# Kernel tuning notes

Hardware: AMD Instinct MI355X
Metric: run time of the kernel (lower is better)

Reference implementation:

```python
import jax, jax.numpy as jnp
import numpy as np

B_, N, C, H = 8192, 49, 192, 6
HD = C // H
SCALE = HD ** -0.5


def setup_inputs() -> dict:
    key = jax.random.key(0)
    k0, k1, k2, k3 = jax.random.split(key, 4)
    x = jax.random.normal(k0, (B_, N, C), dtype=jnp.float32)
    mask = jax.random.randint(k1, (B_, N), 0, 2, dtype=jnp.int32)
    w_qkv = jax.random.normal(k2, (C, 3 * C), dtype=jnp.float32) * 0.02
    b_qkv = jnp.zeros((3 * C,), dtype=jnp.float32)
    w_proj = jax.random.normal(k3, (C, C), dtype=jnp.float32) * 0.02
    b_proj = jnp.zeros((C,), dtype=jnp.float32)
    return {"x": x, "mask": mask, "w_qkv": w_qkv, "b_qkv": b_qkv,
            "w_proj": w_proj, "b_proj": b_proj}


def reference(x, mask, w_qkv, b_qkv, w_proj, b_proj):
    # qkv projection: [B_, N, 3C] -> [3, B_, H, N, HD]
    qkv = (x @ w_qkv + b_qkv).reshape(B_, N, 3, H, HD).transpose(2, 0, 3, 1, 4)
    q, k, v = qkv[0], qkv[1], qkv[2]
    # scaled QK^T: [B_, H, N, N]
    attn = jnp.einsum('bhnd,bhmd->bhnm', q, k) * SCALE
    # additive key mask: mask==0 positions get -inf
    attn = jnp.where(mask[:, None, None, :] == 0, -jnp.inf, attn)
    p = jax.nn.softmax(attn, axis=-1)  # dropout p=0 -> identity
    out = jnp.einsum('bhnm,bhmd->bhnd', p, v)  # AV
    out = out.transpose(0, 2, 1, 3).reshape(B_, N, C)
    return out @ w_proj + b_proj
```

## Files before the change

kernel.cpp:

```cpp
#include <hip/hip_runtime.h>


typedef __attribute__((ext_vector_type(8))) short short8;
typedef __attribute__((ext_vector_type(4))) float f32x4;

#define SCALE 0.17677669529663687f

__device__ __forceinline__ unsigned short f2bf(float x) {
    union { float f; unsigned int i; } v; v.f = x;
    return (unsigned short)((v.i + 0x7FFFu + ((v.i >> 16) & 1u)) >> 16);
}

__device__ __forceinline__ unsigned int pkbf(float lo, float hi) {
    unsigned int r;
    asm("v_cvt_pk_bf16_f32 %0, %1, %2" : "=v"(r) : "v"(lo), "v"(hi));
    return r;
}

__device__ __forceinline__ short8 cvt8(f32x4 lo, f32x4 hi) {
    union { short8 s; unsigned int u[4]; } r;
    r.u[0] = pkbf(lo[0], lo[1]);
    r.u[1] = pkbf(lo[2], lo[3]);
    r.u[2] = pkbf(hi[0], hi[1]);
    r.u[3] = pkbf(hi[2], hi[3]);
    return r.s;
}

__device__ __forceinline__ f32x4 addb(f32x4 v, float b) {
    v[0] += b; v[1] += b; v[2] += b; v[3] += b;
    return v;
}

__device__ __forceinline__ short8 xpose(f32x4 tlo, f32x4 thi, int srcA, bool hi) {
    unsigned int pl0 = pkbf(tlo[0], tlo[1]);
    unsigned int pl1 = pkbf(tlo[2], tlo[3]);
    unsigned int ph0 = pkbf(thi[0], thi[1]);
    unsigned int ph1 = pkbf(thi[2], thi[3]);
    unsigned int a0 = (unsigned int)__shfl((int)pl0, srcA);
    unsigned int b0 = (unsigned int)__shfl((int)ph0, srcA);
    unsigned int a1 = (unsigned int)__shfl((int)pl1, srcA);
    unsigned int b1 = (unsigned int)__shfl((int)ph1, srcA);
    unsigned int a2 = (unsigned int)__shfl((int)pl0, srcA + 16);
    unsigned int b2 = (unsigned int)__shfl((int)ph0, srcA + 16);
    unsigned int a3 = (unsigned int)__shfl((int)pl1, srcA + 16);
    unsigned int b3 = (unsigned int)__shfl((int)ph1, srcA + 16);
    union { short8 s8; unsigned int u[4]; } f;
    f.u[0] = hi ? b0 : a0;
    f.u[1] = hi ? b1 : a1;
    f.u[2] = hi ? b2 : a2;
    f.u[3] = hi ? b3 : a3;
    return f.s8;
}

__global__ void repack_kernel(const float* __restrict__ wqkv,
                              const float* __restrict__ wproj,
                              unsigned short* __restrict__ wq_pack,
                              unsigned short* __restrict__ wp_pack) {
    int idx = blockIdx.x * 256 + threadIdx.x;
    if (idx < 6 * 576 * 32) {
        int kk  = idx & 31;
        int col = (idx >> 5) % 576;
        int kt  = idx / (576 * 32);
        wq_pack[idx] = f2bf(wqkv[(kt * 32 + kk) * 576 + col]);
    } else {
        int j = idx - 6 * 576 * 32;
        if (j < 6 * 192 * 32) {
            int kk  = j & 31;
            int col = (j >> 5) % 192;
            int kt  = j / (192 * 32);
            wp_pack[j] = f2bf(wproj[(kt * 32 + kk) * 192 + col]);
        }
    }
}

__global__ __launch_bounds__(384)
void win_attn_kernel(const float* __restrict__ x,
                     const int* __restrict__ mask,
                     const float* __restrict__ bqkv,
                     const float* __restrict__ bproj,
                     const unsigned short* __restrict__ wq,
                     const unsigned short* __restrict__ wpj,
                     float* __restrict__ out) {
    __shared__ __align__(16) unsigned short region[25600];
    __shared__ __align__(16) float mbias[64];

    const int b    = blockIdx.x;
    const int tid  = threadIdx.x;
    const int lane = tid & 63;
    const int h    = tid >> 6;
    const int quad = lane >> 4;
    const int l16  = lane & 15;

    int colb[6];
    #pragma unroll
    for (int t = 0; t < 6; ++t) colb[t] = (t >> 1) * 192 + h * 32 + (t & 1) * 16;

    const float* xb = x + (size_t)b * 9408;
    for (int i4 = tid; i4 < 2352; i4 += 384) {
        int flat = i4 * 4;
        int n = flat / 192, c = flat % 192;
        float4 v = *(const float4*)(const void*)&xb[flat];
        uint2 pk;
        pk.x = pkbf(v.x, v.y);
        pk.y = pkbf(v.z, v.w);
        *(uint2*)(void*)&region[n * 200 + c] = pk;
    }
    if (tid < 375) {
        uint4 z = {0u, 0u, 0u, 0u};
        *(uint4*)(void*)&region[9800 + tid * 8] = z;
    }
    if (tid < 64)
        mbias[tid] = (tid < 49 && mask[b * 49 + tid] != 0) ? 0.0f : -1e30f;

    short8 bw0[6];
    #pragma unroll
    for (int t = 0; t < 6; ++t)
        bw0[t] = *(const short8*)(const void*)
                 &wq[(size_t)(colb[t] + l16) * 32 + quad * 8];

    __syncthreads();

    const int  srcA = ((lane & 16) << 1) | l16;
    const bool hiq  = (lane & 32) != 0;

    f32x4 acc[6][4];
    #pragma unroll
    for (int t = 0; t < 6; ++t)
        #pragma unroll
        for (int mt = 0; mt < 4; ++mt)
            acc[t][mt] = (f32x4){0.f, 0.f, 0.f, 0.f};

    #pragma unroll
    for (int kt = 0; kt < 6; ++kt) {
        short8 af[4];
        #pragma unroll
        for (int mt = 0; mt < 4; ++mt)
            af[mt] = *(const short8*)(const void*)
                     &region[(mt * 16 + l16) * 200 + kt * 32 + quad * 8];
        #pragma unroll
        for (int t = 0; t < 6; ++t) {
            short8 bw = (kt == 0) ? bw0[t]
                      : *(const short8*)(const void*)
                        &wq[(size_t)(kt * 576 + colb[t] + l16) * 32 + quad * 8];
            #pragma unroll
            for (int mt = 0; mt < 4; ++mt) {
                if (t < 4)
                    acc[t][mt] = __builtin_amdgcn_mfma_f32_16x16x32_bf16(
                                     bw, af[mt], acc[t][mt], 0, 0, 0);
                else
                    acc[t][mt] = __builtin_amdgcn_mfma_f32_16x16x32_bf16(
                                     af[mt], bw, acc[t][mt], 0, 0, 0);
            }
        }
    }

    short8 qf[4], kf[4], vf[2][2];
    {
        f32x4 bq0 = *(const f32x4*)(const void*)&bqkv[colb[0] + quad * 4];
        f32x4 bq1 = *(const f32x4*)(const void*)&bqkv[colb[1] + quad * 4];
        f32x4 bk0 = *(const f32x4*)(const void*)&bqkv[colb[2] + quad * 4];
        f32x4 bk1 = *(const f32x4*)(const void*)&bqkv[colb[3] + quad * 4];
        #pragma unroll
        for (int nt = 0; nt < 4; ++nt) {
            qf[nt] = xpose(acc[0][nt] + bq0, acc[1][nt] + bq1, srcA, hiq);
            kf[nt] = xpose(acc[2][nt] + bk0, acc[3][nt] + bk1, srcA, hiq);
        }
        float bv0 = bqkv[colb[4] + l16];
        float bv1 = bqkv[colb[5] + l16];
        #pragma unroll
        for (int j = 0; j < 2; ++j) {
            vf[0][j] = cvt8(addb(acc[4][2 * j], bv0), addb(acc[4][2 * j + 1], bv0));
            vf[1][j] = cvt8(addb(acc[5][2 * j], bv1), addb(acc[5][2 * j + 1], bv1));
        }
    }

    f32x4 mb4[4];
    #pragma unroll
    for (int mt = 0; mt < 4; ++mt)
        mb4[mt] = *(const f32x4*)(const void*)&mbias[mt * 16 + quad * 4];

    unsigned short* ob = &region[12800];
    #pragma unroll
    for (int nt = 0; nt < 4; ++nt) {
        f32x4 sr[4];
        #pragma unroll
        for (int mt = 0; mt < 4; ++mt) {
            sr[mt] = (f32x4){0.f, 0.f, 0.f, 0.f};
            sr[mt] = __builtin_amdgcn_mfma_f32_16x16x32_bf16(
                         kf[mt], qf[nt], sr[mt], 0, 0, 0);
        }
        float pm[4];
        #pragma unroll
        for (int mt = 0; mt < 4; ++mt) {
            #pragma unroll
            for (int r = 0; r < 4; ++r)
                sr[mt][r] = sr[mt][r] * SCALE + mb4[mt][r];
            pm[mt] = fmaxf(fmaxf(sr[mt][0], sr[mt][1]),
                           fmaxf(sr[mt][2], sr[mt][3]));
        }
        float mx = fmaxf(fmaxf(pm[0], pm[1]), fmaxf(pm[2], pm[3]));
        mx = fmaxf(mx, __shfl_xor(mx, 16));
        mx = fmaxf(mx, __shfl_xor(mx, 32));
        float ps[4];
        #pragma unroll
        for (int mt = 0; mt < 4; ++mt) {
            #pragma unroll
            for (int r = 0; r < 4; ++r)
                sr[mt][r] = __expf(sr[mt][r] - mx);
            ps[mt] = (sr[mt][0] + sr[mt][1]) + (sr[mt][2] + sr[mt][3]);
        }
        float sum = (ps[0] + ps[1]) + (ps[2] + ps[3]);
        sum += __shfl_xor(sum, 16);
        sum += __shfl_xor(sum, 32);
        float inv = 1.0f / sum;
        #pragma unroll
        for (int mt = 0; mt < 4; ++mt)
            #pragma unroll
            for (int r = 0; r < 4; ++r)
                sr[mt][r] *= inv;

        short8 pf[2];
        pf[0] = cvt8(sr[0], sr[1]);
        pf[1] = cvt8(sr[2], sr[3]);

        f32x4 on[2];
        #pragma unroll
        for (int t = 0; t < 2; ++t)
            on[t] = (f32x4){0.f, 0.f, 0.f, 0.f};
        #pragma unroll
        for (int j = 0; j < 2; ++j)
            #pragma unroll
            for (int t = 0; t < 2; ++t)
                on[t] = __builtin_amdgcn_mfma_f32_16x16x32_bf16(
                            pf[j], vf[t][j], on[t], 0, 0, 0);

        #pragma unroll
        for (int t = 0; t < 2; ++t)
            #pragma unroll
            for (int r = 0; r < 4; ++r)
                ob[(nt * 16 + quad * 4 + r) * 200 + h * 32 + t * 16 + l16]
                    = f2bf(on[t][r]);
    }

    short8 bwp[6][2];
    #pragma unroll
    for (int kt = 0; kt < 6; ++kt)
        #pragma unroll
        for (int nt = 0; nt < 2; ++nt)
            bwp[kt][nt] = *(const short8*)(const void*)
                          &wpj[(size_t)(kt * 192 + h * 32 + nt * 16 + l16) * 32
                               + quad * 8];

    __syncthreads();

    f32x4 po[2][4];
    #pragma unroll
    for (int nt = 0; nt < 2; ++nt)
        #pragma unroll
        for (int mt = 0; mt < 4; ++mt)
            po[nt][mt] = (f32x4){0.f, 0.f, 0.f, 0.f};

    #pragma unroll
    for (int kt = 0; kt < 6; ++kt) {
        short8 ao[4];
        #pragma unroll
        for (int mt = 0; mt < 4; ++mt)
            ao[mt] = *(const short8*)(const void*)
                     &ob[(mt * 16 + l16) * 200 + kt * 32 + quad * 8];
        #pragma unroll
        for (int nt = 0; nt < 2; ++nt)
            #pragma unroll
            for (int mt = 0; mt < 4; ++mt)
                po[nt][mt] = __builtin_amdgcn_mfma_f32_16x16x32_bf16(
                                 ao[mt], bwp[kt][nt], po[nt][mt], 0, 0, 0);
    }

    #pragma unroll
    for (int nt = 0; nt < 2; ++nt) {
        int col = h * 32 + nt * 16 + l16;
        float bv = bproj[col];
        #pragma unroll
        for (int mt = 0; mt < 4; ++mt)
            #pragma unroll
            for (int r = 0; r < 4; ++r) {
                int row = mt * 16 + quad * 4 + r;
                if (row < 49)
                    out[(size_t)b * 9408 + row * 192 + col] = po[nt][mt][r] + bv;
            }
    }
}

extern "C" void kernel_launch(void* const* d_in, const int* in_sizes, int n_in,
                              void* d_out, int out_size, void* d_ws, size_t ws_size,
                              hipStream_t stream) {
    const float* x      = (const float*)d_in[0];
    const int*   mask   = (const int*)d_in[1];
    const float* w_qkv  = (const float*)d_in[2];
    const float* b_qkv  = (const float*)d_in[3];
    const float* w_proj = (const float*)d_in[4];
    const float* b_proj = (const float*)d_in[5];
    float*       out    = (float*)d_out;

    unsigned short* wq_pack = (unsigned short*)d_ws;
    unsigned short* wp_pack = wq_pack + 110592;

    repack_kernel<<<(110592 + 36864 + 255) / 256, 256, 0, stream>>>(
        w_qkv, w_proj, wq_pack, wp_pack);
    win_attn_kernel<<<8192, 384, 0, stream>>>(x, mask, b_qkv, b_proj,
                                              wq_pack, wp_pack, out);
}
```

Before: 819.1 us.

## Process eight windows per block with double-buffered prefetch of next window input

Each block now loops over eight windows instead of one, with double-buffered LDS for the bf16 input tile, attention output, and mask bias. The next window's x and mask are loaded into registers after the QKV GEMM and written to the alternate buffer during attention, so global load latency overlaps compute. It also amortises block launch and setup. In exchange, LDS per block roughly doubles, which lowers occupancy, register pressure rises from the staged float4s, and the grid shrinks to 1024 blocks.

```diff
diff --git a/kernel.cpp b/kernel.cpp
--- a/kernel.cpp
+++ b/kernel.cpp
@@ -5,6 +5,7 @@
 typedef __attribute__((ext_vector_type(4))) float f32x4;
 
 #define SCALE 0.17677669529663687f
+#define WPB   8
 
 __device__ __forceinline__ unsigned short f2bf(float x) {
     union { float f; unsigned int i; } v; v.f = x;
@@ -81,212 +82,258 @@
                      const unsigned short* __restrict__ wq,
                      const unsigned short* __restrict__ wpj,
                      float* __restrict__ out) {
-    __shared__ __align__(16) unsigned short region[25600];
-    __shared__ __align__(16) float mbias[64];
-
-    const int b    = blockIdx.x;
+    __shared__ __align__(16) unsigned short xbuf[2][12800];
+    __shared__ __align__(16) unsigned short obuf[2][12800];
+    __shared__ __align__(16) float mbias[2][64];
+
     const int tid  = threadIdx.x;
     const int lane = tid & 63;
     const int h    = tid >> 6;
     const int quad = lane >> 4;
     const int l16  = lane & 15;
+    const int b0   = blockIdx.x * WPB;
+
+    const int  srcA = ((lane & 16) << 1) | l16;
+    const bool hiq  = (lane & 32) != 0;
 
     int colb[6];
     #pragma unroll
     for (int t = 0; t < 6; ++t) colb[t] = (t >> 1) * 192 + h * 32 + (t & 1) * 16;
 
-    const float* xb = x + (size_t)b * 9408;
-    for (int i4 = tid; i4 < 2352; i4 += 384) {
-        int flat = i4 * 4;
-        int n = flat / 192, c = flat % 192;
-        float4 v = *(const float4*)(const void*)&xb[flat];
-        uint2 pk;
-        pk.x = pkbf(v.x, v.y);
-        pk.y = pkbf(v.z, v.w);
-        *(uint2*)(void*)&region[n * 200 + c] = pk;
+    {
+        const float* xb = x + (size_t)b0 * 9408;
+        for (int i4 = tid; i4 < 2352; i4 += 384) {
+            int flat = i4 * 4;
+            int n = flat / 192, c = flat % 192;
+            float4 v = *(const float4*)(const void*)&xb[flat];
+            uint2 pk;
+            pk.x = pkbf(v.x, v.y);
+            pk.y = pkbf(v.z, v.w);
+            *(uint2*)(void*)&xbuf[0][n * 200 + c] = pk;
+        }
+        if (tid < 375) {
+            uint4 z = {0u, 0u, 0u, 0u};
+            *(uint4*)(void*)&xbuf[0][9800 + tid * 8] = z;
+            *(uint4*)(void*)&xbuf[1][9800 + tid * 8] = z;
+        }
+        if (tid < 64)
+            mbias[0][tid] = (tid < 49 && mask[b0 * 49 + tid] != 0) ? 0.0f
+                                                                   : -1e30f;
     }
-    if (tid < 375) {
-        uint4 z = {0u, 0u, 0u, 0u};
-        *(uint4*)(void*)&region[9800 + tid * 8] = z;
-    }
-    if (tid < 64)
-        mbias[tid] = (tid < 49 && mask[b * 49 + tid] != 0) ? 0.0f : -1e30f;
-
-    short8 bw0[6];
-    #pragma unroll
-    for (int t = 0; t < 6; ++t)
-        bw0[t] = *(const short8*)(const void*)
-                 &wq[(size_t)(colb[t] + l16) * 32 + quad * 8];
-
     __syncthreads();
 
-    const int  srcA = ((lane & 16) << 1) | l16;
-    const bool hiq  = (lane & 32) != 0;
-
-    f32x4 acc[6][4];
-    #pragma unroll
-    for (int t = 0; t < 6; ++t)
+    #pragma unroll 1
+    for (int wi = 0; wi < WPB; ++wi) {
+        const int  c    = wi & 1;
+        const int  b    = b0 + wi;
+        const bool more = (wi + 1 < WPB);
+        unsigned short* rg = &xbuf[c][0];
+        unsigned short* ob = &obuf[c][0];
+
+        f32x4 acc[6][4];
+        #pragma unroll
+        for (int t = 0; t < 6; ++t)
+            #pragma unroll
+            for (int mt = 0; mt < 4; ++mt)
+                acc[t][mt] = (f32x4){0.f, 0.f, 0.f, 0.f};
+
+        #pragma unroll
+        for (int kt = 0; kt < 6; ++kt) {
+            short8 af[4];
+            #pragma unroll
+            for (int mt = 0; mt < 4; ++mt)
+                af[mt] = *(const short8*)(const void*)
+                         &rg[(mt * 16 + l16) * 200 + kt * 32 + quad * 8];
+            #pragma unroll
+            for (int t = 0; t < 6; ++t) {
+                short8 bw = *(const short8*)(const void*)
+                            &wq[(size_t)(kt * 576 + colb[t] + l16) * 32 + quad * 8];
+                #pragma unroll
+                for (int mt = 0; mt < 4; ++mt) {
+                    if (t < 4)
+                        acc[t][mt] = __builtin_amdgcn_mfma_f32_16x16x32_bf16(
+                                         bw, af[mt], acc[t][mt], 0, 0, 0);
+                    else
+                        acc[t][mt] = __builtin_amdgcn_mfma_f32_16x16x32_bf16(
+                                         af[mt], bw, acc[t][mt], 0, 0, 0);
+                }
+            }
+        }
+
+        short8 qf[4], kf[4], vf[2][2];
+        {
+            f32x4 bq0 = *(const f32x4*)(const void*)&bqkv[colb[0] + quad * 4];
+            f32x4 bq1 = *(const f32x4*)(const void*)&bqkv[colb[1] + quad * 4];
+            f32x4 bk0 = *(const f32x4*)(const void*)&bqkv[colb[2] + quad * 4];
+            f32x4 bk1 = *(const f32x4*)(const void*)&bqkv[colb[3] + quad * 4];
+            #pragma unroll
+            for (int nt = 0; nt < 4; ++nt) {
+                qf[nt] = xpose(acc[0][nt] + bq0, acc[1][nt] + bq1, srcA, hiq);
+                kf[nt] = xpose(acc[2][nt] + bk0, acc[3][nt] + bk1, srcA, hiq);
+            }
+            float bv0 = bqkv[colb[4] + l16];
+            float bv1 = bqkv[colb[5] + l16];
+            #pragma unroll
+            for (int j = 0; j < 2; ++j) {
+                vf[0][j] = cvt8(addb(acc[4][2 * j], bv0),
+                                addb(acc[4][2 * j + 1], bv0));
+                vf[1][j] = cvt8(addb(acc[5][2 * j], bv1),
+                                addb(acc[5][2 * j + 1], bv1));
+            }
+        }
+
+        __builtin_amdgcn_sched_barrier(0);
+        float4 st[6];
+        float4 st6 = {0.f, 0.f, 0.f, 0.f};
+        int mv = 0;
+        if (more) {
+            const float* xn = x + (size_t)(b + 1) * 9408;
+            #pragma unroll
+            for (int k = 0; k < 6; ++k)
+                st[k] = *(const float4*)(const void*)&xn[(tid + k * 384) * 4];
+            if (tid < 48)
+                st6 = *(const float4*)(const void*)&xn[(2304 + tid) * 4];
+            if (tid < 49)
+                mv = mask[(b + 1) * 49 + tid];
+        }
+
+        f32x4 mb4[4];
         #pragma unroll
         for (int mt = 0; mt < 4; ++mt)
-            acc[t][mt] = (f32x4){0.f, 0.f, 0.f, 0.f};
-
-    #pragma unroll
-    for (int kt = 0; kt < 6; ++kt) {
-        short8 af[4];
-        #pragma unroll
-        for (int mt = 0; mt < 4; ++mt)
-            af[mt] = *(const short8*)(const void*)
-                     &region[(mt * 16 + l16) * 200 + kt * 32 + quad * 8];
-        #pragma unroll
-        for (int t = 0; t < 6; ++t) {
-            short8 bw = (kt == 0) ? bw0[t]
-                      : *(const short8*)(const void*)
-                        &wq[(size_t)(kt * 576 + colb[t] + l16) * 32 + quad * 8];
+            mb4[mt] = *(const f32x4*)(const void*)&mbias[c][mt * 16 + quad * 4];
+
+        #pragma unroll
+        for (int nt = 0; nt < 4; ++nt) {
+            f32x4 sr[4];
             #pragma unroll
             for (int mt = 0; mt < 4; ++mt) {
-                if (t < 4)
-                    acc[t][mt] = __builtin_amdgcn_mfma_f32_16x16x32_bf16(
-                                     bw, af[mt], acc[t][mt], 0, 0, 0);
-                else
-                    acc[t][mt] = __builtin_amdgcn_mfma_f32_16x16x32_bf16(
-                                     af[mt], bw, acc[t][mt], 0, 0, 0);
-            }
-        }
-    }
-
-    short8 qf[4], kf[4], vf[2][2];
-    {
-        f32x4 bq0 = *(const f32x4*)(const void*)&bqkv[colb[0] + quad * 4];
-        f32x4 bq1 = *(const f32x4*)(const void*)&bqkv[colb[1] + quad * 4];
-        f32x4 bk0 = *(const f32x4*)(const void*)&bqkv[colb[2] + quad * 4];
-        f32x4 bk1 = *(const f32x4*)(const void*)&bqkv[colb[3] + quad * 4];
-        #pragma unroll
-        for (int nt = 0; nt < 4; ++nt) {
-            qf[nt] = xpose(acc[0][nt] + bq0, acc[1][nt] + bq1, srcA, hiq);
-            kf[nt] = xpose(acc[2][nt] + bk0, acc[3][nt] + bk1, srcA, hiq);
-        }
-        float bv0 = bqkv[colb[4] + l16];
-        float bv1 = bqkv[colb[5] + l16];
-        #pragma unroll
-        for (int j = 0; j < 2; ++j) {
-            vf[0][j] = cvt8(addb(acc[4][2 * j], bv0), addb(acc[4][2 * j + 1], bv0));
-            vf[1][j] = cvt8(addb(acc[5][2 * j], bv1), addb(acc[5][2 * j + 1], bv1));
-        }
-    }
-
-    f32x4 mb4[4];
-    #pragma unroll
-    for (int mt = 0; mt < 4; ++mt)
-        mb4[mt] = *(const f32x4*)(const void*)&mbias[mt * 16 + quad * 4];
-
-    unsigned short* ob = &region[12800];
-    #pragma unroll
-    for (int nt = 0; nt < 4; ++nt) {
-        f32x4 sr[4];
-        #pragma unroll
-        for (int mt = 0; mt < 4; ++mt) {
-            sr[mt] = (f32x4){0.f, 0.f, 0.f, 0.f};
-            sr[mt] = __builtin_amdgcn_mfma_f32_16x16x32_bf16(
-                         kf[mt], qf[nt], sr[mt], 0, 0, 0);
-        }
-        float pm[4];
-        #pragma unroll
-        for (int mt = 0; mt < 4; ++mt) {
-            #pragma unroll
-            for (int r = 0; r < 4; ++r)
-                sr[mt][r] = sr[mt][r] * SCALE + mb4[mt][r];
-            pm[mt] = fmaxf(fmaxf(sr[mt][0], sr[mt][1]),
-                           fmaxf(sr[mt][2], sr[mt][3]));
-        }
-        float mx = fmaxf(fmaxf(pm[0], pm[1]), fmaxf(pm[2], pm[3]));
-        mx = fmaxf(mx, __shfl_xor(mx, 16));
-        mx = fmaxf(mx, __shfl_xor(mx, 32));
-        float ps[4];
-        #pragma unroll
-        for (int mt = 0; mt < 4; ++mt) {
-            #pragma unroll
-            for (int r = 0; r < 4; ++r)
-                sr[mt][r] = __expf(sr[mt][r] - mx);
-            ps[mt] = (sr[mt][0] + sr[mt][1]) + (sr[mt][2] + sr[mt][3]);
-        }
-        float sum = (ps[0] + ps[1]) + (ps[2] + ps[3]);
-        sum += __shfl_xor(sum, 16);
-        sum += __shfl_xor(sum, 32);
-        float inv = 1.0f / sum;
-        #pragma unroll
-        for (int mt = 0; mt < 4; ++mt)
-            #pragma unroll
-            for (int r = 0; r < 4; ++r)
-                sr[mt][r] *= inv;
-
-        short8 pf[2];
-        pf[0] = cvt8(sr[0], sr[1]);
-        pf[1] = cvt8(sr[2], sr[3]);
-
-        f32x4 on[2];
-        #pragma unroll
-        for (int t = 0; t < 2; ++t)
-            on[t] = (f32x4){0.f, 0.f, 0.f, 0.f};
-        #pragma unroll
-        for (int j = 0; j < 2; ++j)
+                sr[mt] = (f32x4){0.f, 0.f, 0.f, 0.f};
+                sr[mt] = __builtin_amdgcn_mfma_f32_16x16x32_bf16(
+                             kf[mt], qf[nt], sr[mt], 0, 0, 0);
+            }
+            float pm[4];
+            #pragma unroll
+            for (int mt = 0; mt < 4; ++mt) {
+                #pragma unroll
+                for (int r = 0; r < 4; ++r)
+                    sr[mt][r] = sr[mt][r] * SCALE + mb4[mt][r];
+                pm[mt] = fmaxf(fmaxf(sr[mt][0], sr[mt][1]),
+                               fmaxf(sr[mt][2], sr[mt][3]));
+            }
+            float mx = fmaxf(fmaxf(pm[0], pm[1]), fmaxf(pm[2], pm[3]));
+            mx = fmaxf(mx, __shfl_xor(mx, 16));
+            mx = fmaxf(mx, __shfl_xor(mx, 32));
+            float ps[4];
+            #pragma unroll
+            for (int mt = 0; mt < 4; ++mt) {
+                #pragma unroll
+                for (int r = 0; r < 4; ++r)
+                    sr[mt][r] = __expf(sr[mt][r] - mx);
+                ps[mt] = (sr[mt][0] + sr[mt][1]) + (sr[mt][2] + sr[mt][3]);
+            }
+            float sum = (ps[0] + ps[1]) + (ps[2] + ps[3]);
+            sum += __shfl_xor(sum, 16);
+            sum += __shfl_xor(sum, 32);
+            float inv = 1.0f / sum;
+            #pragma unroll
+            for (int mt = 0; mt < 4; ++mt)
+                #pragma unroll
+                for (int r = 0; r < 4; ++r)
+                    sr[mt][r] *= inv;
+
+            short8 pf[2];
+            pf[0] = cvt8(sr[0], sr[1]);
+            pf[1] = cvt8(sr[2], sr[3]);
+
+            f32x4 on[2];
             #pragma unroll
             for (int t = 0; t < 2; ++t)
-                on[t] = __builtin_amdgcn_mfma_f32_16x16x32_bf16(
-                            pf[j], vf[t][j], on[t], 0, 0, 0);
-
-        #pragma unroll
-        for (int t = 0; t < 2; ++t)
-            #pragma unroll
-            for (int r = 0; r < 4; ++r)
-                ob[(nt * 16 + quad * 4 + r) * 200 + h * 32 + t * 16 + l16]
-                    = f2bf(on[t][r]);
-    }
-
-    short8 bwp[6][2];
-    #pragma unroll
-    for (int kt = 0; kt < 6; ++kt)
+                on[t] = (f32x4){0.f, 0.f, 0.f, 0.f};
+            #pragma unroll
+            for (int j = 0; j < 2; ++j)
+                #pragma unroll
+                for (int t = 0; t < 2; ++t)
+                    on[t] = __builtin_amdgcn_mfma_f32_16x16x32_bf16(
+                                pf[j], vf[t][j], on[t], 0, 0, 0);
+
+            #pragma unroll
+            for (int t = 0; t < 2; ++t)
+                #pragma unroll
+                for (int r = 0; r < 4; ++r)
+                    ob[(nt * 16 + quad * 4 + r) * 200 + h * 32 + t * 16 + l16]
+                        = f2bf(on[t][r]);
+        }
+
+        if (more) {
+            unsigned short* nb = &xbuf[c ^ 1][0];
+            #pragma unroll
+            for (int k = 0; k < 6; ++k) {
+                int flat = (tid + k * 384) * 4;
+                int n = flat / 192, cc = flat % 192;
+                uint2 pk;
+                pk.x = pkbf(st[k].x, st[k].y);
+                pk.y = pkbf(st[k].z, st[k].w);
+                *(uint2*)(void*)&nb[n * 200 + cc] = pk;
+            }
+            if (tid < 48) {
+                int flat = (2304 + tid) * 4;
+                int n = flat / 192, cc = flat % 192;
+                uint2 pk;
+                pk.x = pkbf(st6.x, st6.y);
+                pk.y = pkbf(st6.z, st6.w);
+                *(uint2*)(void*)&nb[n * 200 + cc] = pk;
+            }
+            if (tid < 64)
+                mbias[c ^ 1][tid] = (tid < 49 && mv != 0) ? 0.0f : -1e30f;
+        }
+
+        short8 bwp[6][2];
+        #pragma unroll
+        for (int kt = 0; kt < 6; ++kt)
+            #pragma unroll
+            for (int nt = 0; nt < 2; ++nt)
+                bwp[kt][nt] = *(const short8*)(const void*)
+                              &wpj[(size_t)(kt * 192 + h * 32 + nt * 16 + l16) * 32
+                                   + quad * 8];
+
+        __syncthreads();
+
+        f32x4 po[2][4];
         #pragma unroll
         for (int nt = 0; nt < 2; ++nt)
-            bwp[kt][nt] = *(const short8*)(const void*)
-                          &wpj[(size_t)(kt * 192 + h * 32 + nt * 16 + l16) * 32
-                               + quad * 8];
-
-    __syncthreads();
-
-    f32x4 po[2][4];
-    #pragma unroll
-    for (int nt = 0; nt < 2; ++nt)
-        #pragma unroll
-        for (int mt = 0; mt < 4; ++mt)
-            po[nt][mt] = (f32x4){0.f, 0.f, 0.f, 0.f};
-
-    #pragma unroll
-    for (int kt = 0; kt < 6; ++kt) {
-        short8 ao[4];
-        #pragma unroll
-        for (int mt = 0; mt < 4; ++mt)
-            ao[mt] = *(const short8*)(const void*)
-                     &ob[(mt * 16 + l16) * 200 + kt * 32 + quad * 8];
-        #pragma unroll
-        for (int nt = 0; nt < 2; ++nt)
-            #pragma unroll
-            for (int mt = 0; mt < 4; ++mt)
-                po[nt][mt] = __builtin_amdgcn_mfma_f32_16x16x32_bf16(
-                                 ao[mt], bwp[kt][nt], po[nt][mt], 0, 0, 0);
-    }
-
-    #pragma unroll
-    for (int nt = 0; nt < 2; ++nt) {
-        int col = h * 32 + nt * 16 + l16;
-        float bv = bproj[col];
-        #pragma unroll
-        for (int mt = 0; mt < 4; ++mt)
-            #pragma unroll
-            for (int r = 0; r < 4; ++r) {
-                int row = mt * 16 + quad * 4 + r;
-                if (row < 49)
-                    out[(size_t)b * 9408 + row * 192 + col] = po[nt][mt][r] + bv;
-            }
+            #pragma unroll
+            for (int mt = 0; mt < 4; ++mt)
+                po[nt][mt] = (f32x4){0.f, 0.f, 0.f, 0.f};
+
+        #pragma unroll
+        for (int kt = 0; kt < 6; ++kt) {
+            short8 ao[4];
+            #pragma unroll
+            for (int mt = 0; mt < 4; ++mt)
+                ao[mt] = *(const short8*)(const void*)
+                         &ob[(mt * 16 + l16) * 200 + kt * 32 + quad * 8];
+            #pragma unroll
+            for (int nt = 0; nt < 2; ++nt)
+                #pragma unroll
+                for (int mt = 0; mt < 4; ++mt)
+                    po[nt][mt] = __builtin_amdgcn_mfma_f32_16x16x32_bf16(
+                                     ao[mt], bwp[kt][nt], po[nt][mt], 0, 0, 0);
+        }
+
+        #pragma unroll
+        for (int nt = 0; nt < 2; ++nt) {
+            int col = h * 32 + nt * 16 + l16;
+            float bv = bproj[col];
+            #pragma unroll
+            for (int mt = 0; mt < 4; ++mt)
+                #pragma unroll
+                for (int r = 0; r < 4; ++r) {
+                    int row = mt * 16 + quad * 4 + r;
+                    if (row < 49)
+                        out[(size_t)b * 9408 + row * 192 + col]
+                            = po[nt][mt][r] + bv;
+                }
+        }
     }
 }
 
@@ -306,6 +353,6 @@
 
     repack_kernel<<<(110592 + 36864 + 255) / 256, 256, 0, stream>>>(
         w_qkv, w_proj, wq_pack, wp_pack);
-    win_attn_kernel<<<8192, 384, 0, stream>>>(x, mask, b_qkv, b_proj,
-                                              wq_pack, wp_pack, out);
-}
+    win_attn_kernel<<<8192 / WPB, 384, 0, stream>>>(x, mask, b_qkv, b_proj,
+                                                    wq_pack, wp_pack, out);
+}
```

New measurement: 1.241 ms. +51.5%, slower.

## Load x and mask directly from global into MFMA fragments, dropping LDS staging

Applied to the files above, without the earlier changes.

Removes the cooperative staging of x into shared memory (with bf16 conversion), the mask-bias LDS table and the first __syncthreads. Each wave now reads its A fragments for the QKV GEMM straight from global memory and converts them in registers, and reads mask values directly. This shrinks LDS use, which may allow more resident blocks, and removes a barrier. The cost is that every one of the six head-waves re-reads the full x tile from global/L2, about six times the traffic, with strided fp32 loads sitting on the GEMM's critical path.

```diff
diff --git a/kernel.cpp b/kernel.cpp
--- a/kernel.cpp
+++ b/kernel.cpp
@@ -81,8 +81,7 @@
                      const unsigned short* __restrict__ wq,
                      const unsigned short* __restrict__ wpj,
                      float* __restrict__ out) {
-    __shared__ __align__(16) unsigned short region[25600];
-    __shared__ __align__(16) float mbias[64];
+    __shared__ __align__(16) unsigned short ob[12800];
 
     const int b    = blockIdx.x;
     const int tid  = threadIdx.x;
@@ -91,38 +90,15 @@
     const int quad = lane >> 4;
     const int l16  = lane & 15;
 
-    int colb[6];
-    #pragma unroll
-    for (int t = 0; t < 6; ++t) colb[t] = (t >> 1) * 192 + h * 32 + (t & 1) * 16;
-
-    const float* xb = x + (size_t)b * 9408;
-    for (int i4 = tid; i4 < 2352; i4 += 384) {
-        int flat = i4 * 4;
-        int n = flat / 192, c = flat % 192;
-        float4 v = *(const float4*)(const void*)&xb[flat];
-        uint2 pk;
-        pk.x = pkbf(v.x, v.y);
-        pk.y = pkbf(v.z, v.w);
-        *(uint2*)(void*)&region[n * 200 + c] = pk;
-    }
-    if (tid < 375) {
-        uint4 z = {0u, 0u, 0u, 0u};
-        *(uint4*)(void*)&region[9800 + tid * 8] = z;
-    }
-    if (tid < 64)
-        mbias[tid] = (tid < 49 && mask[b * 49 + tid] != 0) ? 0.0f : -1e30f;
-
-    short8 bw0[6];
-    #pragma unroll
-    for (int t = 0; t < 6; ++t)
-        bw0[t] = *(const short8*)(const void*)
-                 &wq[(size_t)(colb[t] + l16) * 32 + quad * 8];
-
-    __syncthreads();
-
     const int  srcA = ((lane & 16) << 1) | l16;
     const bool hiq  = (lane & 32) != 0;
 
+    int colb[6];
+    #pragma unroll
+    for (int t = 0; t < 6; ++t) colb[t] = (t >> 1) * 192 + h * 32 + (t & 1) * 16;
+
+    const float* xb = x + (size_t)b * 9408;
+
     f32x4 acc[6][4];
     #pragma unroll
     for (int t = 0; t < 6; ++t)
@@ -134,13 +110,20 @@
     for (int kt = 0; kt < 6; ++kt) {
         short8 af[4];
         #pragma unroll
-        for (int mt = 0; mt < 4; ++mt)
-            af[mt] = *(const short8*)(const void*)
-                     &region[(mt * 16 + l16) * 200 + kt * 32 + quad * 8];
+        for (int mt = 0; mt < 4; ++mt) {
+            int row = mt * 16 + l16;
+            f32x4 lo = (f32x4){0.f, 0.f, 0.f, 0.f};
+            f32x4 hi = (f32x4){0.f, 0.f, 0.f, 0.f};
+            if (row < 49) {
+                const float* p = &xb[row * 192 + kt * 32 + quad * 8];
+                lo = *(const f32x4*)(const void*)p;
+                hi = *(const f32x4*)(const void*)(p + 4);
+            }
+            af[mt] = cvt8(lo, hi);
+        }
         #pragma unroll
         for (int t = 0; t < 6; ++t) {
-            short8 bw = (kt == 0) ? bw0[t]
-                      : *(const short8*)(const void*)
+            short8 bw = *(const short8*)(const void*)
                         &wq[(size_t)(kt * 576 + colb[t] + l16) * 32 + quad * 8];
             #pragma unroll
             for (int mt = 0; mt < 4; ++mt) {
@@ -177,9 +160,14 @@
     f32x4 mb4[4];
     #pragma unroll
     for (int mt = 0; mt < 4; ++mt)
-        mb4[mt] = *(const f32x4*)(const void*)&mbias[mt * 16 + quad * 4];
-
-    unsigned short* ob = &region[12800];
+        #pragma unroll
+        for (int r = 0; r < 4; ++r) {
+            int row = mt * 16 + quad * 4 + r;
+            int mv = 0;
+            if (row < 49) mv = mask[b * 49 + row];
+            mb4[mt][r] = mv ? 0.0f : -1e30f;
+        }
+
     #pragma unroll
     for (int nt = 0; nt < 4; ++nt) {
         f32x4 sr[4];
```

After: 1.046 ms. 27.7% more time.

## Split each head across two wavefronts and share K/V through LDS

Applied to the files above, without the earlier changes.

The block grows from 6 to 12 wavefronts, with two waves per head, each owning half of the 64 token rows. The QKV GEMM, attention and output projection are all split along rows. K and V fragments are exchanged through new LDS buffers behind an extra barrier, and the x staging region is reused for the attention output. This raises wave-level parallelism and cuts per-wave register pressure. In exchange it duplicates the weight-fragment loads per head, adds a barrier, and increases LDS use per block.

```diff
diff --git a/kernel.cpp b/kernel.cpp
--- a/kernel.cpp
+++ b/kernel.cpp
@@ -73,7 +73,7 @@
     }
 }
 
-__global__ __launch_bounds__(384)
+__global__ __launch_bounds__(768)
 void win_attn_kernel(const float* __restrict__ x,
                      const int* __restrict__ mask,
                      const float* __restrict__ bqkv,
@@ -81,22 +81,29 @@
                      const unsigned short* __restrict__ wq,
                      const unsigned short* __restrict__ wpj,
                      float* __restrict__ out) {
-    __shared__ __align__(16) unsigned short region[25600];
+    __shared__ __align__(16) unsigned short region[12800];
+    __shared__ __align__(16) short8 kfb[6][4][64];
+    __shared__ __align__(16) short8 vfb[6][2][2][64];
     __shared__ __align__(16) float mbias[64];
 
     const int b    = blockIdx.x;
     const int tid  = threadIdx.x;
     const int lane = tid & 63;
-    const int h    = tid >> 6;
+    const int w    = tid >> 6;
+    const int h    = w >> 1;
+    const int m    = w & 1;
     const int quad = lane >> 4;
     const int l16  = lane & 15;
 
+    const int  srcA = ((lane & 16) << 1) | l16;
+    const bool hiq  = (lane & 32) != 0;
+
     int colb[6];
     #pragma unroll
     for (int t = 0; t < 6; ++t) colb[t] = (t >> 1) * 192 + h * 32 + (t & 1) * 16;
 
     const float* xb = x + (size_t)b * 9408;
-    for (int i4 = tid; i4 < 2352; i4 += 384) {
+    for (int i4 = tid; i4 < 2352; i4 += 768) {
         int flat = i4 * 4;
         int n = flat / 192, c = flat % 192;
         float4 v = *(const float4*)(const void*)&xb[flat];
@@ -120,74 +127,79 @@
 
     __syncthreads();
 
-    const int  srcA = ((lane & 16) << 1) | l16;
-    const bool hiq  = (lane & 32) != 0;
-
-    f32x4 acc[6][4];
+    f32x4 acc[6][2];
     #pragma unroll
     for (int t = 0; t < 6; ++t)
         #pragma unroll
-        for (int mt = 0; mt < 4; ++mt)
-            acc[t][mt] = (f32x4){0.f, 0.f, 0.f, 0.f};
+        for (int i = 0; i < 2; ++i)
+            acc[t][i] = (f32x4){0.f, 0.f, 0.f, 0.f};
 
     #pragma unroll
     for (int kt = 0; kt < 6; ++kt) {
-        short8 af[4];
-        #pragma unroll
-        for (int mt = 0; mt < 4; ++mt)
-            af[mt] = *(const short8*)(const void*)
-                     &region[(mt * 16 + l16) * 200 + kt * 32 + quad * 8];
+        short8 af[2];
+        #pragma unroll
+        for (int i = 0; i < 2; ++i)
+            af[i] = *(const short8*)(const void*)
+                    &region[((2 * m + i) * 16 + l16) * 200 + kt * 32 + quad * 8];
         #pragma unroll
         for (int t = 0; t < 6; ++t) {
             short8 bw = (kt == 0) ? bw0[t]
                       : *(const short8*)(const void*)
                         &wq[(size_t)(kt * 576 + colb[t] + l16) * 32 + quad * 8];
             #pragma unroll
-            for (int mt = 0; mt < 4; ++mt) {
+            for (int i = 0; i < 2; ++i) {
                 if (t < 4)
-                    acc[t][mt] = __builtin_amdgcn_mfma_f32_16x16x32_bf16(
-                                     bw, af[mt], acc[t][mt], 0, 0, 0);
+                    acc[t][i] = __builtin_amdgcn_mfma_f32_16x16x32_bf16(
+                                    bw, af[i], acc[t][i], 0, 0, 0);
                 else
-                    acc[t][mt] = __builtin_amdgcn_mfma_f32_16x16x32_bf16(
-                                     af[mt], bw, acc[t][mt], 0, 0, 0);
+                    acc[t][i] = __builtin_amdgcn_mfma_f32_16x16x32_bf16(
+                                    af[i], bw, acc[t][i], 0, 0, 0);
             }
         }
     }
 
-    short8 qf[4], kf[4], vf[2][2];
+    short8 qf[2];
     {
         f32x4 bq0 = *(const f32x4*)(const void*)&bqkv[colb[0] + quad * 4];
         f32x4 bq1 = *(const f32x4*)(const void*)&bqkv[colb[1] + quad * 4];
         f32x4 bk0 = *(const f32x4*)(const void*)&bqkv[colb[2] + quad * 4];
         f32x4 bk1 = *(const f32x4*)(const void*)&bqkv[colb[3] + quad * 4];
         #pragma unroll
-        for (int nt = 0; nt < 4; ++nt) {
-            qf[nt] = xpose(acc[0][nt] + bq0, acc[1][nt] + bq1, srcA, hiq);
-            kf[nt] = xpose(acc[2][nt] + bk0, acc[3][nt] + bk1, srcA, hiq);
+        for (int i = 0; i < 2; ++i) {
+            qf[i] = xpose(acc[0][i] + bq0, acc[1][i] + bq1, srcA, hiq);
+            kfb[h][2 * m + i][lane]
+                = xpose(acc[2][i] + bk0, acc[3][i] + bk1, srcA, hiq);
         }
         float bv0 = bqkv[colb[4] + l16];
         float bv1 = bqkv[colb[5] + l16];
-        #pragma unroll
-        for (int j = 0; j < 2; ++j) {
-            vf[0][j] = cvt8(addb(acc[4][2 * j], bv0), addb(acc[4][2 * j + 1], bv0));
-            vf[1][j] = cvt8(addb(acc[5][2 * j], bv1), addb(acc[5][2 * j + 1], bv1));
-        }
-    }
+        vfb[h][0][m][lane] = cvt8(addb(acc[4][0], bv0), addb(acc[4][1], bv0));
+        vfb[h][1][m][lane] = cvt8(addb(acc[5][0], bv1), addb(acc[5][1], bv1));
+    }
+
+    __syncthreads();
+
+    short8 kf[4], vf[2][2];
+    #pragma unroll
+    for (int mt = 0; mt < 4; ++mt) kf[mt] = kfb[h][mt][lane];
+    #pragma unroll
+    for (int t = 0; t < 2; ++t)
+        #pragma unroll
+        for (int j = 0; j < 2; ++j) vf[t][j] = vfb[h][t][j][lane];
 
     f32x4 mb4[4];
     #pragma unroll
     for (int mt = 0; mt < 4; ++mt)
         mb4[mt] = *(const f32x4*)(const void*)&mbias[mt * 16 + quad * 4];
 
-    unsigned short* ob = &region[12800];
-    #pragma unroll
-    for (int nt = 0; nt < 4; ++nt) {
+    #pragma unroll
+    for (int i = 0; i < 2; ++i) {
+        const int nt = 2 * m + i;
         f32x4 sr[4];
         #pragma unroll
         for (int mt = 0; mt < 4; ++mt) {
             sr[mt] = (f32x4){0.f, 0.f, 0.f, 0.f};
             sr[mt] = __builtin_amdgcn_mfma_f32_16x16x32_bf16(
-                         kf[mt], qf[nt], sr[mt], 0, 0, 0);
+                         kf[mt], qf[i], sr[mt], 0, 0, 0);
         }
         float pm[4];
         #pragma unroll
@@ -238,7 +250,7 @@
         for (int t = 0; t < 2; ++t)
             #pragma unroll
             for (int r = 0; r < 4; ++r)
-                ob[(nt * 16 + quad * 4 + r) * 200 + h * 32 + t * 16 + l16]
+                region[(nt * 16 + quad * 4 + r) * 200 + h * 32 + t * 16 + l16]
                     = f2bf(on[t][r]);
     }
 
@@ -253,26 +265,26 @@
 
     __syncthreads();
 
-    f32x4 po[2][4];
+    f32x4 po[2][2];
     #pragma unroll
     for (int nt = 0; nt < 2; ++nt)
         #pragma unroll
-        for (int mt = 0; mt < 4; ++mt)
-            po[nt][mt] = (f32x4){0.f, 0.f, 0.f, 0.f};
+        for (int i = 0; i < 2; ++i)
+            po[nt][i] = (f32x4){0.f, 0.f, 0.f, 0.f};
 
     #pragma unroll
     for (int kt = 0; kt < 6; ++kt) {
-        short8 ao[4];
-        #pragma unroll
-        for (int mt = 0; mt < 4; ++mt)
-            ao[mt] = *(const short8*)(const void*)
-                     &ob[(mt * 16 + l16) * 200 + kt * 32 + quad * 8];
+        short8 ao[2];
+        #pragma unroll
+        for (int i = 0; i < 2; ++i)
+            ao[i] = *(const short8*)(const void*)
+                    &region[((2 * m + i) * 16 + l16) * 200 + kt * 32 + quad * 8];
         #pragma unroll
         for (int nt = 0; nt < 2; ++nt)
             #pragma unroll
-            for (int mt = 0; mt < 4; ++mt)
-                po[nt][mt] = __builtin_amdgcn_mfma_f32_16x16x32_bf16(
-                                 ao[mt], bwp[kt][nt], po[nt][mt], 0, 0, 0);
+            for (int i = 0; i < 2; ++i)
+                po[nt][i] = __builtin_amdgcn_mfma_f32_16x16x32_bf16(
+                                ao[i], bwp[kt][nt], po[nt][i], 0, 0, 0);
     }
 
     #pragma unroll
@@ -280,12 +292,12 @@
         int col = h * 32 + nt * 16 + l16;
         float bv = bproj[col];
         #pragma unroll
-        for (int mt = 0; mt < 4; ++mt)
+        for (int i = 0; i < 2; ++i)
             #pragma unroll
             for (int r = 0; r < 4; ++r) {
-                int row = mt * 16 + quad * 4 + r;
+                int row = (2 * m + i) * 16 + quad * 4 + r;
                 if (row < 49)
-                    out[(size_t)b * 9408 + row * 192 + col] = po[nt][mt][r] + bv;
+                    out[(size_t)b * 9408 + row * 192 + col] = po[nt][i][r] + bv;
             }
     }
 }
@@ -306,6 +318,6 @@
 
     repack_kernel<<<(110592 + 36864 + 255) / 256, 256, 0, stream>>>(
         w_qkv, w_proj, wq_pack, wp_pack);
-    win_attn_kernel<<<8192, 384, 0, stream>>>(x, mask, b_qkv, b_proj,
+    win_attn_kernel<<<8192, 768, 0, stream>>>(x, mask, b_qkv, b_proj,
                                               wq_pack, wp_pack, out);
 }
```

Measured after the change: 825.1 us. No clear change (+0.7%).
